# Kernel tuning notes

Measured on AMD Instinct MI355X. Metric: run time of the kernel, lower is better.

The kernel has to match this reference:

```python
import jax, jax.numpy as jnp
import numpy as np

D_MODEL, N_STATE, L_MAX, BATCH = 256, 64, 2048, 16

def _to_c(x):
    return jax.lax.complex(x[..., 0], x[..., 1])

def setup_inputs() -> dict:
    key = jax.random.key(0)
    k_u, k_ct_r, k_ct_i, k_step = jax.random.split(key, 4)
    n, d = N_STATE, D_MODEL
    # --- HiPPO DPLR init (numpy, matches torch hippo_dplr) ---
    P = np.sqrt(1.0 + 2.0 * np.arange(1, n + 1, dtype=np.float64))
    A = np.tril(np.outer(P, P)) - np.diag(np.arange(1, n + 1, dtype=np.float64))
    A = -A
    p = 0.5 * np.sqrt(2.0 * np.arange(1, n + 1, dtype=np.float64) + 1.0)
    Ap = (A + np.outer(p, p)).astype(np.complex64)
    lam, V = np.linalg.eig(Ap)
    p_rot = V.conj().T @ p.astype(np.complex64)
    p_ri = np.stack([p_rot.real, p_rot.imag], -1).astype(np.float32)          # (n,2)
    lambda_ri = np.stack([lam.real, lam.imag], -1).astype(np.float32)         # (n,2)
    # --- B init: sqrt(2k+1), repeated over channels, zero imag ---
    B_r = np.sqrt(2.0 * np.arange(1, n + 1) + 1.0).astype(np.float32)
    B_ri = np.stack([np.tile(B_r, (d, 1)), np.zeros((d, n), np.float32)], -1) # (d,n,2)
    # --- Ct: xavier-normal complex ---
    std = float(np.sqrt(2.0 / (d + n)))
    Ct_r = jax.random.normal(k_ct_r, (d, n), jnp.float32) * (std / np.sqrt(2.0))
    Ct_i = jax.random.normal(k_ct_i, (d, n), jnp.float32) * (std / np.sqrt(2.0))
    Ct_ri = jnp.stack([Ct_r, Ct_i], -1)                                        # (d,n,2)
    Dp = jnp.ones((1, 1, d), jnp.float32)
    log_step = jax.random.uniform(k_step, (d,), jnp.float32) * (
        np.log(0.1) - np.log(0.001)) + np.log(0.001)
    u = jax.random.normal(k_u, (BATCH, L_MAX, d), jnp.float32)
    return {"u": u, "p_ri": jnp.asarray(p_ri), "lambda_ri": jnp.asarray(lambda_ri),
            "B_ri": jnp.asarray(B_ri), "Ct_ri": Ct_ri, "Dp": Dp, "log_step": log_step}

def reference(u, p_ri, lambda_ri, B_ri, Ct_ri, Dp, log_step):
    p = _to_c(p_ri)          # (n,)
    lam = _to_c(lambda_ri)   # (n,)
    B = _to_c(B_ri)          # (d,n)
    Ct = _to_c(Ct_ri)        # (d,n)
    L = u.shape[1]
    omega = jnp.exp(2j * jnp.pi * jnp.arange(L) / L).astype(jnp.complex64)  # (L,)
    step = jnp.exp(log_step)                                               # (d,)
    g = (2.0 / step)[:, None] * ((1.0 - omega) / (1.0 + omega))[None, :]   # (d,L)
    c = 2.0 / (1.0 + omega)                                                # (L,)
    inv = 1.0 / (g[:, :, None] - lam[None, None, :])                       # (d,L,n)
    k00 = jnp.einsum('dn,dln->dl', Ct.conj() * B, inv)
    k01 = jnp.einsum('dn,dln->dl', Ct.conj() * p[None, :], inv)
    k10 = jnp.einsum('dn,dln->dl', p.conj()[None, :] * B, inv)
    k11 = jnp.einsum('n,dln->dl', p.conj() * p, inv)
    at_roots = c[None, :] * (k00 - k01 * k10 / (1.0 + k11))                # (d,L)
    out = jnp.fft.ifft(at_roots, n=L, axis=-1)
    order = jnp.concatenate([jnp.zeros((1,), jnp.int32), jnp.arange(L - 1, 0, -1)])
    K = out[:, order].real[None]                                           # (1,d,L)
    # causal FFT convolution
    ud = jnp.fft.rfft(jnp.pad(u, ((0, 0), (0, L), (0, 0))), axis=1)        # (B,L+1,d)
    Kd = jnp.fft.rfft(jnp.pad(K, ((0, 0), (0, 0), (0, L))), axis=-1)       # (1,d,L+1)
    y = jnp.fft.irfft(jnp.transpose(ud, (0, 2, 1)) * Kd, axis=-1)[..., :L]
    y = jnp.transpose(y, (0, 2, 1)).astype(u.dtype)                        # (B,L,d)
    return y + Dp * u
```

## Files before the change

kernel.cpp:

```cpp
#include <hip/hip_runtime.h>
#include <math.h>

#define LLEN   2048
#define NFFT   4096
#define DMODEL 256
#define NSTATE 64
#define NBATCH 16
#define PI_F   3.14159265358979323846f

#define PADIDX(a) ((a) + ((a) >> 4))
#define LDSN  (NFFT + (NFFT >> 4))
#define LDSN2 (LLEN + (LLEN >> 4))
#define KSTRIDE 2056

__device__ inline float frcp(float x) { return __builtin_amdgcn_rcpf(x); }

#define RADIX4(ar0,ai0,ar1,ai1,ar2,ai2,ar3,ai3,S) do {                      \
    float s0r=(ar0)+(ar2), s0i=(ai0)+(ai2);                                 \
    float s1r=(ar0)-(ar2), s1i=(ai0)-(ai2);                                 \
    float s2r=(ar1)+(ar3), s2i=(ai1)+(ai3);                                 \
    float s3r=(ar1)-(ar3), s3i=(ai1)-(ai3);                                 \
    (ar0)=s0r+s2r; (ai0)=s0i+s2i;                                           \
    (ar2)=s0r-s2r; (ai2)=s0i-s2i;                                           \
    (ar1)=s1r-(S)*s3i; (ai1)=s1i+(S)*s3r;                                   \
    (ar3)=s1r+(S)*s3i; (ai3)=s1i-(S)*s3r;                                   \
} while (0)

template<int SIGN>
__device__ inline void dft16(float xr[16], float xi[16]) {
    const float S = (float)SIGN;
    const float C1 = 0.9238795325112867f, S1 = 0.3826834323650898f;
    const float C2 = 0.7071067811865476f;
    RADIX4(xr[0],xi[0], xr[4],xi[4], xr[8],xi[8],  xr[12],xi[12], S);
    RADIX4(xr[1],xi[1], xr[5],xi[5], xr[9],xi[9],  xr[13],xi[13], S);
    RADIX4(xr[2],xi[2], xr[6],xi[6], xr[10],xi[10],xr[14],xi[14], S);
    RADIX4(xr[3],xi[3], xr[7],xi[7], xr[11],xi[11],xr[15],xi[15], S);
#define TW(idx, wr_, wi_) { float tr = xr[idx]*(wr_) - xi[idx]*(wi_);       \
    xi[idx] = xr[idx]*(wi_) + xi[idx]*(wr_); xr[idx] = tr; }
    TW(5,  C1,  S*S1);
    TW(6,  C2,  S*C2);
    TW(7,  S1,  S*C1);
    TW(9,  C2,  S*C2);
    TW(10, 0.f, S);
    TW(11, -C2, S*C2);
    TW(13, S1,  S*C1);
    TW(14, -C2, S*C2);
    TW(15, -C1, -S*S1);
#undef TW
    RADIX4(xr[0],xi[0],  xr[1],xi[1],  xr[2],xi[2],  xr[3],xi[3],  S);
    RADIX4(xr[4],xi[4],  xr[5],xi[5],  xr[6],xi[6],  xr[7],xi[7],  S);
    RADIX4(xr[8],xi[8],  xr[9],xi[9],  xr[10],xi[10],xr[11],xi[11],S);
    RADIX4(xr[12],xi[12],xr[13],xi[13],xr[14],xi[14],xr[15],xi[15],S);
}

template<int SIGN>
__device__ inline void dft8(float xr[8], float xi[8]) {
    const float S = (float)SIGN;
    const float C2 = 0.7071067811865476f;
    RADIX4(xr[0],xi[0], xr[2],xi[2], xr[4],xi[4], xr[6],xi[6], S);
    RADIX4(xr[1],xi[1], xr[3],xi[3], xr[5],xi[5], xr[7],xi[7], S);
    { float tr = xr[3]*C2 - xi[3]*(S*C2); xi[3] = xr[3]*(S*C2) + xi[3]*C2; xr[3] = tr; }
    { float tr = -S*xi[5]; xi[5] = S*xr[5]; xr[5] = tr; }
    { float tr = xr[7]*(-C2) - xi[7]*(S*C2); xi[7] = xr[7]*(S*C2) + xi[7]*(-C2); xr[7] = tr; }
    float br[8], bi[8];
#pragma unroll
    for (int k = 0; k < 4; ++k) {
        br[k]   = xr[2*k] + xr[2*k+1]; bi[k]   = xi[2*k] + xi[2*k+1];
        br[k+4] = xr[2*k] - xr[2*k+1]; bi[k+4] = xi[2*k] - xi[2*k+1];
    }
#pragma unroll
    for (int k = 0; k < 8; ++k) { xr[k] = br[k]; xi[k] = bi[k]; }
}

template<int SIGN>
__device__ inline void tw_apply16(float xr[16], float xi[16], float ang) {
    float wr[16], wi[16];
    __sincosf(ang, &wi[1], &wr[1]);
#pragma unroll
    for (int k = 1; k < 8; ++k) {
        wr[2*k]   = wr[k]*wr[k] - wi[k]*wi[k];
        wi[2*k]   = 2.f * wr[k] * wi[k];
        wr[2*k+1] = wr[k]*wr[k+1] - wi[k]*wi[k+1];
        wi[2*k+1] = wr[k]*wi[k+1] + wi[k]*wr[k+1];
    }
#pragma unroll
    for (int t = 1; t < 16; ++t) {
        float tr = xr[t]*wr[t] - xi[t]*wi[t];
        xi[t] = xr[t]*wi[t] + xi[t]*wr[t];
        xr[t] = tr;
    }
}

template<int SIGN, int M, int L, bool PRUNE>
__device__ inline void stage16(float2* X, int j, bool active) {
    float xr[16], xi[16];
    const int p = j & (L - 1);
    if (active) {
#pragma unroll
        for (int t = 0; t < 16; ++t) {
            float2 v = X[PADIDX(j + t * M)];
            xr[t] = v.x; xi[t] = v.y;
        }
        tw_apply16<SIGN>(xr, xi, ((float)SIGN * 2.f * PI_F / (float)(16 * L)) * (float)p);
        dft16<SIGN>(xr, xi);
    }
    __syncthreads();
    if (active) {
        const int base = 16 * j - 15 * p;
#pragma unroll
        for (int k0 = 0; k0 < 4; ++k0)
#pragma unroll
            for (int k2 = 0; k2 < 4; ++k2) {
                const int u = k0 + 4 * k2;
                if (!PRUNE || u < 8) {
                    const int a = base + u * L;
                    X[PADIDX(a)] = make_float2(xr[4*k0+k2], xi[4*k0+k2]);
                }
            }
    }
    __syncthreads();
}

template<int SIGN, bool ZHI, bool PRUNE>
__device__ inline void fft4096_f2(float2* X, int tid) {
    float xr[16], xi[16];
#pragma unroll
    for (int t = 0; t < 16; ++t) {
        if (ZHI && t >= 8) { xr[t] = 0.f; xi[t] = 0.f; }
        else { float2 v = X[PADIDX(tid + t * 256)]; xr[t] = v.x; xi[t] = v.y; }
    }
    dft16<SIGN>(xr, xi);
    __syncthreads();
#pragma unroll
    for (int k0 = 0; k0 < 4; ++k0)
#pragma unroll
        for (int k2 = 0; k2 < 4; ++k2)
            X[PADIDX(16 * tid + k0 + 4 * k2)] = make_float2(xr[4*k0+k2], xi[4*k0+k2]);
    __syncthreads();
    stage16<SIGN, 256, 16,  false>(X, tid, true);
    stage16<SIGN, 256, 256, PRUNE>(X, tid, true);
}

template<int SIGN>
__device__ inline void fft2048_f2(float2* X, int tid) {
    float xr[8], xi[8];
#pragma unroll
    for (int t = 0; t < 8; ++t) {
        float2 v = X[PADIDX(tid + t * 256)];
        xr[t] = v.x; xi[t] = v.y;
    }
    dft8<SIGN>(xr, xi);
    __syncthreads();
#pragma unroll
    for (int u = 0; u < 8; ++u)
        X[PADIDX(8 * tid + u)] = make_float2(xr[u], xi[u]);
    __syncthreads();
    stage16<SIGN, 128, 8,   false>(X, tid, tid < 128);
    stage16<SIGN, 128, 128, false>(X, tid, tid < 128);
}

__global__ __launch_bounds__(256) void k_ar(const float* __restrict__ p_ri,
                                            const float* __restrict__ lambda_ri,
                                            const float* __restrict__ B_ri,
                                            const float* __restrict__ Ct_ri,
                                            const float* __restrict__ log_step,
                                            float2* __restrict__ ar_out) {
    __shared__ float4 c0[NSTATE], c1[NSTATE];
    __shared__ float2 lam[NSTATE];
    const int d = blockIdx.x >> 1;
    const int lbase = (blockIdx.x & 1) << 10;
    const int tid = threadIdx.x;
    if (tid < NSTATE) {
        const int n = tid;
        const float px = p_ri[2*n], py = p_ri[2*n+1];
        lam[n] = make_float2(lambda_ri[2*n], lambda_ri[2*n+1]);
        const float Bx = B_ri[(d*NSTATE+n)*2], By = B_ri[(d*NSTATE+n)*2+1];
        const float Cx = Ct_ri[(d*NSTATE+n)*2], Cy = Ct_ri[(d*NSTATE+n)*2+1];
        c0[n] = make_float4(Cx*Bx + Cy*By, Cx*By - Cy*Bx,
                            Cx*px + Cy*py, Cx*py - Cy*px);
        c1[n] = make_float4(px*Bx + py*By, px*By - py*Bx, px*px + py*py, 0.f);
    }
    __syncthreads();

    const float tos = 2.f * __expf(-log_step[d]);
    float gx[4], gy[4], ccx[4], ccy[4];
    float k00x[4], k00y[4], k01x[4], k01y[4];
    float k10x[4], k10y[4], k11x[4], k11y[4];
#pragma unroll
    for (int j = 0; j < 4; ++j) {
        const int l = lbase + tid + (j << 8);
        float sn, cs;
        sincosf(2.f * PI_F * (float)l / (float)LLEN, &sn, &cs);
        const float opx = 1.f + cs, opy = sn;
        const float omx = 1.f - cs, omy = -sn;
        const float inv_op = frcp(opx*opx + opy*opy);
        gx[j] = tos * (omx*opx + omy*opy) * inv_op;
        gy[j] = tos * (omy*opx - omx*opy) * inv_op;
        ccx[j] = 2.f * opx * inv_op; ccy[j] = -2.f * opy * inv_op;
        k00x[j]=0.f; k00y[j]=0.f; k01x[j]=0.f; k01y[j]=0.f;
        k10x[j]=0.f; k10y[j]=0.f; k11x[j]=0.f; k11y[j]=0.f;
    }
    for (int n = 0; n < NSTATE; ++n) {
        const float2 lm = lam[n];
        const float4 a = c0[n];
        const float4 b = c1[n];
#pragma unroll
        for (int j = 0; j < 4; ++j) {
            const float dx = gx[j] - lm.x, dy = gy[j] - lm.y;
            const float idn = frcp(dx*dx + dy*dy);
            const float ix = dx * idn, iy = -dy * idn;
            k00x[j] += a.x*ix - a.y*iy;  k00y[j] += a.x*iy + a.y*ix;
            k01x[j] += a.z*ix - a.w*iy;  k01y[j] += a.z*iy + a.w*ix;
            k10x[j] += b.x*ix - b.y*iy;  k10y[j] += b.x*iy + b.y*ix;
            k11x[j] += b.z*ix;           k11y[j] += b.z*iy;
        }
    }
#pragma unroll
    for (int j = 0; j < 4; ++j) {
        const float nx = k01x[j]*k10x[j] - k01y[j]*k10y[j];
        const float ny = k01x[j]*k10y[j] + k01y[j]*k10x[j];
        const float dpx = 1.f + k11x[j], dpy = k11y[j];
        const float idq = frcp(dpx*dpx + dpy*dpy);
        const float qx = (nx*dpx + ny*dpy) * idq;
        const float qy = (ny*dpx - nx*dpy) * idq;
        const float rx = k00x[j] - qx, ry = k00y[j] - qy;
        ar_out[(size_t)d * LLEN + lbase + tid + (j << 8)] =
            make_float2(ccx[j]*rx - ccy[j]*ry, ccx[j]*ry + ccy[j]*rx);
    }
}

__global__ __launch_bounds__(256, 4) void k_mix(const float2* __restrict__ a_in,
                                                float2* __restrict__ Hc) {
    __shared__ float2 X[LDSN2];
    const int tid = threadIdx.x;
    const int d = blockIdx.x;
    const float isc = 1.f / (float)NFFT;
    const float4* a4 = (const float4*)(a_in + (size_t)d * LLEN);
#pragma unroll
    for (int k = 0; k < 4; ++k) {
        const int v = tid + k * 256;
        const float4 w = a4[v];
        X[PADIDX(2 * v)]     = make_float2(w.x, w.y);
        X[PADIDX(2 * v + 1)] = make_float2(w.z, w.w);
    }
    __syncthreads();

    float2* H = Hc + (size_t)d * KSTRIDE;
    for (int m = tid; m <= 1024; m += 256) {
        const float2 am = X[PADIDX(m)];
        const float2 an = X[PADIDX((LLEN - m) & (LLEN - 1))];
        H[2 * m] = make_float2((an.x + am.x) * 0.5f * isc,
                               (an.y - am.y) * 0.5f * isc);
    }
    fft2048_f2<-1>(X, tid);

#pragma unroll
    for (int k = 0; k < 8; ++k) {
        const int j = tid + k * 256;
        const int q = PADIDX(j);
        const float Kj = X[q].x * (1.f / (float)LLEN);
        float snj, csj;
        __sincosf(-PI_F * (float)j * (1.f / 2048.f), &snj, &csj);
        X[q] = make_float2(Kj * csj, Kj * snj);
    }
    __syncthreads();
    fft2048_f2<-1>(X, tid);

    for (int m = tid; m < 1024; m += 256) {
        const float2 w = X[PADIDX(m)];
        H[2 * m + 1] = make_float2(w.x * isc, w.y * isc);
    }
}

__device__ inline void pointwise2(float2* __restrict__ X,
                                  const float2* __restrict__ Ha,
                                  const float2* __restrict__ Hb, int tid) {
    for (int f = tid; f <= NFFT / 2; f += 256) {
        const int fb = (NFFT - f) & (NFFT - 1);
        const float2 Za = X[PADIDX(f)], Zb = X[PADIDX(fb)];
        const float xax = 0.5f * (Za.x + Zb.x), xay = 0.5f * (Za.y - Zb.y);
        const float xbx = 0.5f * (Za.y + Zb.y), xby = -0.5f * (Za.x - Zb.x);
        const float2 A = Ha[f], B = Hb[f];
        const float yax = xax*A.x - xay*A.y, yay = xax*A.y + xay*A.x;
        const float ybx = xbx*B.x - xby*B.y, yby = xbx*B.y + xby*B.x;
        X[PADIDX(f)] = make_float2(yax - yby, yay + ybx);
        if (fb != f)
            X[PADIDX(fb)] = make_float2(yax + yby, ybx - yay);
    }
    __syncthreads();
}

__global__ __launch_bounds__(256, 4) void k_fused(const float* __restrict__ u,
                                                  const float2* __restrict__ Hc,
                                                  const float* __restrict__ Dp,
                                                  float* __restrict__ out) {
    __shared__ float2 X[LDSN];
    const int i = blockIdx.x;
    const int x = i & 7;
    const int s = i >> 3;
    const int b = s >> 3;
    const int q = (x << 3) | (s & 7);
    const int ch = q * 4;
    const int tid = threadIdx.x;

    const float* ub = u + (size_t)b * (LLEN * DMODEL) + ch;
    float2 uvA[8], zB[8];
#pragma unroll
    for (int k = 0; k < 8; ++k) {
        const int t = tid + k * 256;
        const float4 v = *(const float4*)(ub + (size_t)t * DMODEL);
        uvA[k] = make_float2(v.x, v.y);
        zB[k]  = make_float2(v.z, v.w);
        X[PADIDX(t)] = uvA[k];
    }
    __syncthreads();

    fft4096_f2<-1, true, false>(X, tid);
    pointwise2(X, Hc + (size_t)ch * KSTRIDE, Hc + (size_t)(ch + 1) * KSTRIDE, tid);
    fft4096_f2<+1, false, true>(X, tid);

    float2 yA[8];
#pragma unroll
    for (int k = 0; k < 8; ++k) {
        const int t = tid + k * 256;
        yA[k] = X[PADIDX(t)];
        X[PADIDX(t)] = zB[k];
    }
    __syncthreads();

    fft4096_f2<-1, true, false>(X, tid);
    pointwise2(X, Hc + (size_t)(ch + 2) * KSTRIDE, Hc + (size_t)(ch + 3) * KSTRIDE, tid);
    fft4096_f2<+1, false, true>(X, tid);

    const float4 dp = *(const float4*)(Dp + ch);
    float* ob = out + (size_t)b * (LLEN * DMODEL) + ch;
#pragma unroll
    for (int k = 0; k < 8; ++k) {
        const int t = tid + k * 256;
        const float2 yB = X[PADIDX(t)];
        float4 o;
        o.x = yA[k].x + dp.x * uvA[k].x;
        o.y = yA[k].y + dp.y * uvA[k].y;
        o.z = yB.x    + dp.z * zB[k].x;
        o.w = yB.y    + dp.w * zB[k].y;
        *(float4*)(ob + (size_t)t * DMODEL) = o;
    }
}

extern "C" void kernel_launch(void* const* d_in, const int* in_sizes, int n_in,
                              void* d_out, int out_size, void* d_ws, size_t ws_size,
                              hipStream_t stream) {
    const float* u         = (const float*)d_in[0];
    const float* p_ri      = (const float*)d_in[1];
    const float* lambda_ri = (const float*)d_in[2];
    const float* B_ri      = (const float*)d_in[3];
    const float* Ct_ri     = (const float*)d_in[4];
    const float* Dp        = (const float*)d_in[5];
    const float* log_step  = (const float*)d_in[6];
    float* out = (float*)d_out;

    float2* Hc = (float2*)d_ws;
    float2* a  = (float2*)((char*)d_ws + (size_t)DMODEL * KSTRIDE * sizeof(float2));

    k_ar   <<<DMODEL * 2, 256, 0, stream>>>(p_ri, lambda_ri, B_ri, Ct_ri, log_step, a);
    k_mix  <<<DMODEL, 256, 0, stream>>>(a, Hc);
    k_fused<<<NBATCH * (DMODEL / 4), 256, 0, stream>>>(u, Hc, Dp, out);
}
```

Baseline: 184.7 us.

## Split fused conv to two channels per block with XOR-swizzled LDS

Each block now handles one channel pair (one packed complex FFT round trip) instead of four channels processed in two sequential passes, which doubles the grid. The LDS layout switches from padded indexing to an XOR swizzle so the buffer is exactly 4096 float2 (32 KB), and the first FFT starts directly from registers loaded from global memory. Launch bounds are raised to 8 blocks per CU to increase occupancy. The trade-off is that the input is re-read from global in the epilogue instead of being kept in registers, the store width drops to float2, and bank-conflict behaviour changes with the swizzle.

```diff
diff --git a/kernel.cpp b/kernel.cpp
--- a/kernel.cpp
+++ b/kernel.cpp
@@ -9,9 +9,10 @@
 #define PI_F   3.14159265358979323846f
 
 #define PADIDX(a) ((a) + ((a) >> 4))
-#define LDSN  (NFFT + (NFFT >> 4))
 #define LDSN2 (LLEN + (LLEN >> 4))
 #define KSTRIDE 2056
+
+#define SWZIDX(a) ((a) ^ (((a) >> 4) & 15))
 
 __device__ inline float frcp(float x) { return __builtin_amdgcn_rcpf(x); }
 
@@ -121,26 +122,6 @@
     __syncthreads();
 }
 
-template<int SIGN, bool ZHI, bool PRUNE>
-__device__ inline void fft4096_f2(float2* X, int tid) {
-    float xr[16], xi[16];
-#pragma unroll
-    for (int t = 0; t < 16; ++t) {
-        if (ZHI && t >= 8) { xr[t] = 0.f; xi[t] = 0.f; }
-        else { float2 v = X[PADIDX(tid + t * 256)]; xr[t] = v.x; xi[t] = v.y; }
-    }
-    dft16<SIGN>(xr, xi);
-    __syncthreads();
-#pragma unroll
-    for (int k0 = 0; k0 < 4; ++k0)
-#pragma unroll
-        for (int k2 = 0; k2 < 4; ++k2)
-            X[PADIDX(16 * tid + k0 + 4 * k2)] = make_float2(xr[4*k0+k2], xi[4*k0+k2]);
-    __syncthreads();
-    stage16<SIGN, 256, 16,  false>(X, tid, true);
-    stage16<SIGN, 256, 256, PRUNE>(X, tid, true);
-}
-
 template<int SIGN>
 __device__ inline void fft2048_f2(float2* X, int tid) {
     float xr[8], xi[8];
@@ -157,6 +138,66 @@
     __syncthreads();
     stage16<SIGN, 128, 8,   false>(X, tid, tid < 128);
     stage16<SIGN, 128, 128, false>(X, tid, tid < 128);
+}
+
+template<int SIGN, int M, int L, bool PRUNE>
+__device__ inline void stage16s(float2* X, int j) {
+    float xr[16], xi[16];
+    const int p = j & (L - 1);
+#pragma unroll
+    for (int t = 0; t < 16; ++t) {
+        float2 v = X[SWZIDX(j + t * M)];
+        xr[t] = v.x; xi[t] = v.y;
+    }
+    tw_apply16<SIGN>(xr, xi, ((float)SIGN * 2.f * PI_F / (float)(16 * L)) * (float)p);
+    dft16<SIGN>(xr, xi);
+    __syncthreads();
+    const int base = 16 * j - 15 * p;
+#pragma unroll
+    for (int k0 = 0; k0 < 4; ++k0)
+#pragma unroll
+        for (int k2 = 0; k2 < 4; ++k2) {
+            const int u = k0 + 4 * k2;
+            if (!PRUNE || u < 8) {
+                const int a = base + u * L;
+                X[SWZIDX(a)] = make_float2(xr[4*k0+k2], xi[4*k0+k2]);
+            }
+        }
+    __syncthreads();
+}
+
+template<int SIGN, bool PRUNE>
+__device__ inline void fft4096_swz_from_regs(float2* X, int tid,
+                                             float xr[16], float xi[16]) {
+    dft16<SIGN>(xr, xi);
+#pragma unroll
+    for (int k0 = 0; k0 < 4; ++k0)
+#pragma unroll
+        for (int k2 = 0; k2 < 4; ++k2)
+            X[SWZIDX(16 * tid + k0 + 4 * k2)] = make_float2(xr[4*k0+k2], xi[4*k0+k2]);
+    __syncthreads();
+    stage16s<SIGN, 256, 16,  false>(X, tid);
+    stage16s<SIGN, 256, 256, PRUNE>(X, tid);
+}
+
+template<int SIGN, bool PRUNE>
+__device__ inline void fft4096_swz(float2* X, int tid) {
+    float xr[16], xi[16];
+#pragma unroll
+    for (int t = 0; t < 16; ++t) {
+        float2 v = X[SWZIDX(tid + t * 256)];
+        xr[t] = v.x; xi[t] = v.y;
+    }
+    dft16<SIGN>(xr, xi);
+    __syncthreads();
+#pragma unroll
+    for (int k0 = 0; k0 < 4; ++k0)
+#pragma unroll
+        for (int k2 = 0; k2 < 4; ++k2)
+            X[SWZIDX(16 * tid + k0 + 4 * k2)] = make_float2(xr[4*k0+k2], xi[4*k0+k2]);
+    __syncthreads();
+    stage16s<SIGN, 256, 16,  false>(X, tid);
+    stage16s<SIGN, 256, 256, PRUNE>(X, tid);
 }
 
 __global__ __launch_bounds__(256) void k_ar(const float* __restrict__ p_ri,
@@ -272,78 +313,61 @@
     }
 }
 
-__device__ inline void pointwise2(float2* __restrict__ X,
-                                  const float2* __restrict__ Ha,
-                                  const float2* __restrict__ Hb, int tid) {
+__device__ inline void pointwise2s(float2* __restrict__ X,
+                                   const float2* __restrict__ Ha,
+                                   const float2* __restrict__ Hb, int tid) {
     for (int f = tid; f <= NFFT / 2; f += 256) {
         const int fb = (NFFT - f) & (NFFT - 1);
-        const float2 Za = X[PADIDX(f)], Zb = X[PADIDX(fb)];
+        const float2 Za = X[SWZIDX(f)], Zb = X[SWZIDX(fb)];
         const float xax = 0.5f * (Za.x + Zb.x), xay = 0.5f * (Za.y - Zb.y);
         const float xbx = 0.5f * (Za.y + Zb.y), xby = -0.5f * (Za.x - Zb.x);
         const float2 A = Ha[f], B = Hb[f];
         const float yax = xax*A.x - xay*A.y, yay = xax*A.y + xay*A.x;
         const float ybx = xbx*B.x - xby*B.y, yby = xbx*B.y + xby*B.x;
-        X[PADIDX(f)] = make_float2(yax - yby, yay + ybx);
+        X[SWZIDX(f)] = make_float2(yax - yby, yay + ybx);
         if (fb != f)
-            X[PADIDX(fb)] = make_float2(yax + yby, ybx - yay);
-    }
-    __syncthreads();
-}
-
-__global__ __launch_bounds__(256, 4) void k_fused(const float* __restrict__ u,
+            X[SWZIDX(fb)] = make_float2(yax + yby, ybx - yay);
+    }
+    __syncthreads();
+}
+
+__global__ __launch_bounds__(256, 8) void k_fused(const float* __restrict__ u,
                                                   const float2* __restrict__ Hc,
                                                   const float* __restrict__ Dp,
                                                   float* __restrict__ out) {
-    __shared__ float2 X[LDSN];
+    __shared__ float2 X[NFFT];
     const int i = blockIdx.x;
     const int x = i & 7;
     const int s = i >> 3;
-    const int b = s >> 3;
-    const int q = (x << 3) | (s & 7);
-    const int ch = q * 4;
+    const int b  = s >> 4;
+    const int cp = (x << 4) | (s & 15);
+    const int ch = cp * 2;
     const int tid = threadIdx.x;
 
     const float* ub = u + (size_t)b * (LLEN * DMODEL) + ch;
-    float2 uvA[8], zB[8];
+
+    float xr[16], xi[16];
+#pragma unroll
+    for (int k = 0; k < 8; ++k) {
+        const float2 v = *(const float2*)(ub + (size_t)(tid + k * 256) * DMODEL);
+        xr[k] = v.x; xi[k] = v.y;
+    }
+#pragma unroll
+    for (int k = 8; k < 16; ++k) { xr[k] = 0.f; xi[k] = 0.f; }
+
+    fft4096_swz_from_regs<-1, false>(X, tid, xr, xi);
+    pointwise2s(X, Hc + (size_t)ch * KSTRIDE, Hc + (size_t)(ch + 1) * KSTRIDE, tid);
+    fft4096_swz<+1, true>(X, tid);
+
+    const float2 dp = *(const float2*)(Dp + ch);
+    float* ob = out + (size_t)b * (LLEN * DMODEL) + ch;
 #pragma unroll
     for (int k = 0; k < 8; ++k) {
         const int t = tid + k * 256;
-        const float4 v = *(const float4*)(ub + (size_t)t * DMODEL);
-        uvA[k] = make_float2(v.x, v.y);
-        zB[k]  = make_float2(v.z, v.w);
-        X[PADIDX(t)] = uvA[k];
-    }
-    __syncthreads();
-
-    fft4096_f2<-1, true, false>(X, tid);
-    pointwise2(X, Hc + (size_t)ch * KSTRIDE, Hc + (size_t)(ch + 1) * KSTRIDE, tid);
-    fft4096_f2<+1, false, true>(X, tid);
-
-    float2 yA[8];
-#pragma unroll
-    for (int k = 0; k < 8; ++k) {
-        const int t = tid + k * 256;
-        yA[k] = X[PADIDX(t)];
-        X[PADIDX(t)] = zB[k];
-    }
-    __syncthreads();
-
-    fft4096_f2<-1, true, false>(X, tid);
-    pointwise2(X, Hc + (size_t)(ch + 2) * KSTRIDE, Hc + (size_t)(ch + 3) * KSTRIDE, tid);
-    fft4096_f2<+1, false, true>(X, tid);
-
-    const float4 dp = *(const float4*)(Dp + ch);
-    float* ob = out + (size_t)b * (LLEN * DMODEL) + ch;
-#pragma unroll
-    for (int k = 0; k < 8; ++k) {
-        const int t = tid + k * 256;
-        const float2 yB = X[PADIDX(t)];
-        float4 o;
-        o.x = yA[k].x + dp.x * uvA[k].x;
-        o.y = yA[k].y + dp.y * uvA[k].y;
-        o.z = yB.x    + dp.z * zB[k].x;
-        o.w = yB.y    + dp.w * zB[k].y;
-        *(float4*)(ob + (size_t)t * DMODEL) = o;
+        const float2 v  = X[SWZIDX(t)];
+        const float2 uu = *(const float2*)(ub + (size_t)t * DMODEL);
+        *(float2*)(ob + (size_t)t * DMODEL) =
+            make_float2(v.x + dp.x * uu.x, v.y + dp.y * uu.y);
     }
 }
 
@@ -364,5 +388,5 @@
 
     k_ar   <<<DMODEL * 2, 256, 0, stream>>>(p_ri, lambda_ri, B_ri, Ct_ri, log_step, a);
     k_mix  <<<DMODEL, 256, 0, stream>>>(a, Hc);
-    k_fused<<<NBATCH * (DMODEL / 4), 256, 0, stream>>>(u, Hc, Dp, out);
-}
+    k_fused<<<NBATCH * (DMODEL / 2), 256, 0, stream>>>(u, Hc, Dp, out);
+}
```

New measurement: 185.1 us. Within noise of the previous version (+0.2%).
